# Kernel optimization log

Measured on AMD Instinct MI355X. Metric: run time of the kernel, lower is better.

The kernel has to match this reference:

```python
import jax, jax.numpy as jnp
import numpy as np

DIM = 3072
HEADS = 24
HEAD_DIM = 128
INNER = HEADS * HEAD_DIM
EPS = 1e-6
B, IMG_LEN, TXT_LEN = 1, 2048, 512
S = IMG_LEN + TXT_LEN


def setup_inputs() -> dict:
    key = jax.random.key(0)
    ks = jax.random.split(key, 16)
    w = lambda k, shp: (jax.random.normal(k, shp, dtype=jnp.float32) * 0.02)
    return {
        "x": jax.random.normal(ks[0], (B, IMG_LEN, DIM), dtype=jnp.float32),
        "ctx": jax.random.normal(ks[1], (B, TXT_LEN, DIM), dtype=jnp.float32),
        "rope_cos": jax.random.uniform(ks[2], (S, HEAD_DIM), dtype=jnp.float32),
        "rope_sin": jax.random.uniform(ks[3], (S, HEAD_DIM), dtype=jnp.float32),
        "wq": w(ks[4], (INNER, DIM)),
        "wk": w(ks[5], (INNER, DIM)),
        "wv": w(ks[6], (INNER, DIM)),
        "gq": jnp.ones((HEAD_DIM,), jnp.float32),
        "gk": jnp.ones((HEAD_DIM,), jnp.float32),
        "wo": w(ks[7], (DIM, INNER)),
        "awq": w(ks[8], (INNER, DIM)),
        "awk": w(ks[9], (INNER, DIM)),
        "awv": w(ks[10], (INNER, DIM)),
        "agq": jnp.ones((HEAD_DIM,), jnp.float32),
        "agk": jnp.ones((HEAD_DIM,), jnp.float32),
        "awo": w(ks[11], (DIM, INNER)),
    }


def _rms_norm(t, g):
    # t: [b, s, h, d]; normalize over last dim
    var = jnp.mean(t * t, axis=-1, keepdims=True)
    return t * jax.lax.rsqrt(var + EPS) * g


def _heads(t):
    # [b, s, h*d] -> [b, s, h, d]
    b, s, _ = t.shape
    return t.reshape(b, s, HEADS, HEAD_DIM)


def _apply_rope(t, cos, sin):
    # t: [b, s, h, d]; cos/sin: [s, d] interleaved-pair layout (diffusers Flux style)
    b, s, h, d = t.shape
    x = t.reshape(b, s, h, d // 2, 2)
    rot = jnp.stack([-x[..., 1], x[..., 0]], axis=-1).reshape(b, s, h, d)
    c = cos[None, :, None, :]
    si = sin[None, :, None, :]
    return t * c + rot * si


def reference(x, ctx, rope_cos, rope_sin, wq, wk, wv, gq, gk, wo,
              awq, awk, awv, agq, agk, awo):
    # image-stream QKV + per-head RMSNorm on q,k
    q = _rms_norm(_heads(x @ wq.T), gq)
    k = _rms_norm(_heads(x @ wk.T), gk)
    v = _heads(x @ wv.T)
    # context-stream QKV
    qc = _rms_norm(_heads(ctx @ awq.T), agq)
    kc = _rms_norm(_heads(ctx @ awk.T), agk)
    vc = _heads(ctx @ awv.T)
    # joint streams: [ctx, img] ordering (out[:, :txt_len] is context)
    q = jnp.concatenate([qc, q], axis=1)
    k = jnp.concatenate([kc, k], axis=1)
    v = jnp.concatenate([vc, v], axis=1)
    q = _apply_rope(q, rope_cos, rope_sin)
    k = _apply_rope(k, rope_cos, rope_sin)
    # SDPA
    scale = 1.0 / jnp.sqrt(jnp.float32(HEAD_DIM))
    scores = jnp.einsum('bqhd,bkhd->bhqk', q, k) * scale
    probs = jax.nn.softmax(scores, axis=-1)
    out = jnp.einsum('bhqk,bkhd->bqhd', probs, v)
    out = out.reshape(out.shape[0], out.shape[1], INNER)
    img_out = out[:, TXT_LEN:] @ wo.T
    txt_out = out[:, :TXT_LEN] @ awo.T
    return (img_out, txt_out)
```

## Files before the change

kernel.cpp:

```cpp
#include <hip/hip_runtime.h>
#include <hip/hip_bf16.h>

#define DIMC 3072
#define NHEADS 24
#define HD 128
#define SEQ 2560
#define TXTLEN 512
#define IMGLEN 2048

using short8 = __attribute__((ext_vector_type(8))) short;
using f32x4  = __attribute__((ext_vector_type(4))) float;

static __device__ __forceinline__ float bf2f(unsigned short u) {
    unsigned v = ((unsigned)u) << 16;
    return __builtin_bit_cast(float, v);
}
static __device__ __forceinline__ unsigned short f2bf(float f) {
    unsigned u = __builtin_bit_cast(unsigned, f);
    return (unsigned short)((u + 0x7FFFu + ((u >> 16) & 1u)) >> 16);
}
static __device__ __forceinline__ void gload16(const void* g, void* l) {
    __builtin_amdgcn_global_load_lds((const __attribute__((address_space(1))) unsigned int*)g,
                                     (__attribute__((address_space(3))) unsigned int*)l,
                                     16, 0, 0);
}

__global__ __launch_bounds__(256)
void castk(const float* __restrict__ in, unsigned short* __restrict__ out, int n8)
{
    const int i = blockIdx.x * 256 + threadIdx.x;
    if (i >= n8) return;
    const float4 a = *reinterpret_cast<const float4*>(in + (size_t)i * 8);
    const float4 b = *reinterpret_cast<const float4*>(in + (size_t)i * 8 + 4);
    short8 o;
    o[0] = (short)f2bf(a.x); o[1] = (short)f2bf(a.y);
    o[2] = (short)f2bf(a.z); o[3] = (short)f2bf(a.w);
    o[4] = (short)f2bf(b.x); o[5] = (short)f2bf(b.y);
    o[6] = (short)f2bf(b.z); o[7] = (short)f2bf(b.w);
    *reinterpret_cast<short8*>(out + (size_t)i * 8) = o;
}

struct W8 { const float* src[8]; };
__global__ __launch_bounds__(256)
void castw(W8 a, unsigned short* __restrict__ dstbase, int n8, size_t wsz)
{
    const int i = blockIdx.x * 256 + threadIdx.x;
    if (i >= n8) return;
    const float* in = a.src[blockIdx.y];
    unsigned short* out = dstbase + (size_t)blockIdx.y * wsz;
    const float4 av = *reinterpret_cast<const float4*>(in + (size_t)i * 8);
    const float4 bv = *reinterpret_cast<const float4*>(in + (size_t)i * 8 + 4);
    short8 o;
    o[0] = (short)f2bf(av.x); o[1] = (short)f2bf(av.y);
    o[2] = (short)f2bf(av.z); o[3] = (short)f2bf(av.w);
    o[4] = (short)f2bf(bv.x); o[5] = (short)f2bf(bv.y);
    o[6] = (short)f2bf(bv.z); o[7] = (short)f2bf(bv.w);
    *reinterpret_cast<short8*>(out + (size_t)i * 8) = o;
}

struct QkvArgs {
    const unsigned short* A;
    const unsigned short* w0[3];
    const unsigned short* w1[3];
    unsigned short* c[3];
};

__global__ __launch_bounds__(256)
void gemm_qkv(QkvArgs args)
{
    __shared__ unsigned short As[3][128 * 32];
    __shared__ unsigned short Bs[3][128 * 32];

    const int bid = blockIdx.x;
    const int swz = (bid & 7) * 180 + (bid >> 3);
    const int bm = swz % 20;
    int bn = swz / 20;
    const int which = bn / 24; bn -= which * 24;

    const int rowbase = bm * 128, colbase = bn * 128;
    const unsigned short* __restrict__ A = args.A;
    const unsigned short* __restrict__ W = (rowbase < TXTLEN) ? args.w0[which] : args.w1[which];
    unsigned short* __restrict__ C = args.c[which];

    const int t = threadIdx.x, w = t >> 6, l = t & 63;
    const int lr = l & 15, lk = l >> 4;
    const int wr = (w >> 1) * 64, wc = (w & 1) * 64;

    f32x4 acc[4][4] = {};

    const int ssl = ((l & 3) ^ ((l >> 3) & 3)) * 8;
    const unsigned short* Ag = A + (size_t)(rowbase + w * 32 + (l >> 2)) * DIMC + ssl;
    const unsigned short* Wg = W + (size_t)(colbase + w * 32 + (l >> 2)) * DIMC + ssl;

    auto STAGE = [&](int buf, int k0) {
        gload16(Ag + k0,             &As[buf][w * 1024]);
        gload16(Ag + 16 * DIMC + k0, &As[buf][w * 1024 + 512]);
        gload16(Wg + k0,             &Bs[buf][w * 1024]);
        gload16(Wg + 16 * DIMC + k0, &Bs[buf][w * 1024 + 512]);
    };

    constexpr int NIT = DIMC / 32;
    STAGE(0, 0);
    STAGE(1, 32);

    const int rsl = (lk ^ ((lr >> 1) & 3)) * 8;
    int buf = 0;
    for (int it = 0; it < NIT; ++it) {
        asm volatile("s_waitcnt vmcnt(4)" ::: "memory");
        __builtin_amdgcn_s_barrier();
        asm volatile("" ::: "memory");

        {
            const int k2 = (it + 2 < NIT) ? (it + 2) : (NIT - 1);
            int b2 = buf + 2; if (b2 >= 3) b2 -= 3;
            STAGE(b2, k2 * 32);
        }

        short8 af[4], bf[4];
#pragma unroll
        for (int m = 0; m < 4; ++m)
            af[m] = *reinterpret_cast<const short8*>(&As[buf][(wr + m * 16 + lr) * 32 + rsl]);
#pragma unroll
        for (int n = 0; n < 4; ++n)
            bf[n] = *reinterpret_cast<const short8*>(&Bs[buf][(wc + n * 16 + lr) * 32 + rsl]);

        __builtin_amdgcn_s_setprio(1);
#pragma unroll
        for (int m = 0; m < 4; ++m)
#pragma unroll
            for (int n = 0; n < 4; ++n)
                acc[m][n] = __builtin_amdgcn_mfma_f32_16x16x32_bf16(af[m], bf[n], acc[m][n], 0, 0, 0);
        __builtin_amdgcn_s_setprio(0);

        buf = (buf + 1 == 3) ? 0 : buf + 1;
    }

#pragma unroll
    for (int m = 0; m < 4; ++m) {
#pragma unroll
        for (int r = 0; r < 4; ++r) {
            const int row = rowbase + wr + m * 16 + lk * 4 + r;
            unsigned short* crow = C + (size_t)row * DIMC + colbase + wc;
#pragma unroll
            for (int n = 0; n < 4; ++n)
                crow[n * 16 + lr] = f2bf(acc[m][n][r]);
        }
    }
}

__global__ __launch_bounds__(256)
void gemm_out(const unsigned short* __restrict__ A, const unsigned short* __restrict__ W0,
              const unsigned short* __restrict__ W1, float* __restrict__ Ctxt,
              float* __restrict__ Cimg)
{
    __shared__ unsigned short As[3][128 * 32];
    __shared__ unsigned short Bs[3][128 * 32];

    const int bid = blockIdx.x;
    const int swz = (bid & 7) * 60 + (bid >> 3);
    const int bm = swz % 20;
    const int bn = swz / 20;

    const int rowbase = bm * 128, colbase = bn * 128;
    const unsigned short* __restrict__ W = (rowbase < TXTLEN) ? W0 : W1;

    const int t = threadIdx.x, w = t >> 6, l = t & 63;
    const int lr = l & 15, lk = l >> 4;
    const int wr = (w >> 1) * 64, wc = (w & 1) * 64;

    f32x4 acc[4][4] = {};

    const int ssl = ((l & 3) ^ ((l >> 3) & 3)) * 8;
    const unsigned short* Ag = A + (size_t)(rowbase + w * 32 + (l >> 2)) * DIMC + ssl;
    const unsigned short* Wg = W + (size_t)(colbase + w * 32 + (l >> 2)) * DIMC + ssl;

    auto STAGE = [&](int buf, int k0) {
        gload16(Ag + k0,             &As[buf][w * 1024]);
        gload16(Ag + 16 * DIMC + k0, &As[buf][w * 1024 + 512]);
        gload16(Wg + k0,             &Bs[buf][w * 1024]);
        gload16(Wg + 16 * DIMC + k0, &Bs[buf][w * 1024 + 512]);
    };

    constexpr int NIT = DIMC / 32;
    STAGE(0, 0);
    STAGE(1, 32);

    const int rsl = (lk ^ ((lr >> 1) & 3)) * 8;
    int buf = 0;
    for (int it = 0; it < NIT; ++it) {
        asm volatile("s_waitcnt vmcnt(4)" ::: "memory");
        __builtin_amdgcn_s_barrier();
        asm volatile("" ::: "memory");

        {
            const int k2 = (it + 2 < NIT) ? (it + 2) : (NIT - 1);
            int b2 = buf + 2; if (b2 >= 3) b2 -= 3;
            STAGE(b2, k2 * 32);
        }

        short8 af[4], bf[4];
#pragma unroll
        for (int m = 0; m < 4; ++m)
            af[m] = *reinterpret_cast<const short8*>(&As[buf][(wr + m * 16 + lr) * 32 + rsl]);
#pragma unroll
        for (int n = 0; n < 4; ++n)
            bf[n] = *reinterpret_cast<const short8*>(&Bs[buf][(wc + n * 16 + lr) * 32 + rsl]);

        __builtin_amdgcn_s_setprio(1);
#pragma unroll
        for (int m = 0; m < 4; ++m)
#pragma unroll
            for (int n = 0; n < 4; ++n)
                acc[m][n] = __builtin_amdgcn_mfma_f32_16x16x32_bf16(af[m], bf[n], acc[m][n], 0, 0, 0);
        __builtin_amdgcn_s_setprio(0);

        buf = (buf + 1 == 3) ? 0 : buf + 1;
    }

    float* Cb; int rloc;
    if (rowbase < TXTLEN) { Cb = Ctxt; rloc = rowbase; }
    else                  { Cb = Cimg; rloc = rowbase - TXTLEN; }
#pragma unroll
    for (int m = 0; m < 4; ++m) {
#pragma unroll
        for (int r = 0; r < 4; ++r) {
            const int row = rloc + wr + m * 16 + lk * 4 + r;
            float* crow = Cb + (size_t)row * DIMC + colbase + wc;
#pragma unroll
            for (int n = 0; n < 4; ++n)
                crow[n * 16 + lr] = acc[m][n][r];
        }
    }
}

__global__ __launch_bounds__(256)
void normrope(unsigned short* __restrict__ Q, unsigned short* __restrict__ K,
              const float* __restrict__ gq, const float* __restrict__ gk,
              const float* __restrict__ agq, const float* __restrict__ agk,
              const float* __restrict__ rc, const float* __restrict__ rs)
{
    const int wid  = (blockIdx.x << 2) + (threadIdx.x >> 6);
    const int lane = threadIdx.x & 63;
    const int s = wid / NHEADS, h = wid - s * NHEADS;
    const bool img = (s >= TXTLEN);
    const float* gq_ = img ? gq : agq;
    const float* gk_ = img ? gk : agk;

    const size_t base = (size_t)s * DIMC + h * HD + lane * 2;
    const float2 c2  = *reinterpret_cast<const float2*>(rc + (size_t)s * HD + lane * 2);
    const float2 s2  = *reinterpret_cast<const float2*>(rs + (size_t)s * HD + lane * 2);
    const float2 gqv = *reinterpret_cast<const float2*>(gq_ + lane * 2);
    const float2 gkv = *reinterpret_cast<const float2*>(gk_ + lane * 2);

    {
        unsigned pr = *reinterpret_cast<unsigned*>(Q + base);
        float vx = bf2f((unsigned short)(pr & 0xffff));
        float vy = bf2f((unsigned short)(pr >> 16));
        float ss = vx * vx + vy * vy;
#pragma unroll
        for (int off = 1; off < 64; off <<= 1) ss += __shfl_xor(ss, off);
        const float rr = rsqrtf(ss * (1.f / HD) + 1e-6f);
        const float txv = vx * rr * gqv.x, tyv = vy * rr * gqv.y;
        const float qs = 0.08838834764831845f;
        const float ox = (txv * c2.x - tyv * s2.x) * qs;
        const float oy = (tyv * c2.y + txv * s2.y) * qs;
        *reinterpret_cast<unsigned*>(Q + base) = (unsigned)f2bf(ox) | ((unsigned)f2bf(oy) << 16);
    }
    {
        unsigned pr = *reinterpret_cast<unsigned*>(K + base);
        float vx = bf2f((unsigned short)(pr & 0xffff));
        float vy = bf2f((unsigned short)(pr >> 16));
        float ss = vx * vx + vy * vy;
#pragma unroll
        for (int off = 1; off < 64; off <<= 1) ss += __shfl_xor(ss, off);
        const float rr = rsqrtf(ss * (1.f / HD) + 1e-6f);
        const float txv = vx * rr * gkv.x, tyv = vy * rr * gkv.y;
        const float ox = txv * c2.x - tyv * s2.x;
        const float oy = tyv * c2.y + txv * s2.y;
        *reinterpret_cast<unsigned*>(K + base) = (unsigned)f2bf(ox) | ((unsigned)f2bf(oy) << 16);
    }
}

__global__ __launch_bounds__(256)
void transpose_v(const unsigned short* __restrict__ V, unsigned short* __restrict__ Vt)
{
    __shared__ unsigned short Ts[64][136];
    const int kt = blockIdx.x, h = blockIdx.y;
    const int t = threadIdx.x;
#pragma unroll
    for (int p = 0; p < 4; ++p) {
        const int row = p * 16 + (t >> 4);
        const int col = (t & 15) * 8;
        *reinterpret_cast<short8*>(&Ts[row][col]) =
            *reinterpret_cast<const short8*>(V + (size_t)(kt * 64 + row) * DIMC + h * HD + col);
    }
    __syncthreads();
    const int d = t >> 1, kh = t & 1;
    unsigned short* dst = Vt + (size_t)h * HD * SEQ + (size_t)d * SEQ + kt * 64 + kh * 32;
#pragma unroll
    for (int j4 = 0; j4 < 4; ++j4) {
        short8 o;
#pragma unroll
        for (int j = 0; j < 8; ++j) o[j] = (short)Ts[kh * 32 + j4 * 8 + j][d];
        *reinterpret_cast<short8*>(dst + j4 * 8) = o;
    }
}

__global__ __launch_bounds__(512)
void attn_mfma(const unsigned short* __restrict__ Q, const unsigned short* __restrict__ K,
               const unsigned short* __restrict__ Vt, unsigned short* __restrict__ O)
{
    __shared__ unsigned short Ks[2][64 * 128];
    __shared__ unsigned short Vs[2][128 * 64];
    __shared__ unsigned short Ps[8][16 * 64];

    const int bid = blockIdx.x;
    const int swz = (bid & 7) * 60 + (bid >> 3);
    const int bq = swz % 20;
    const int h  = swz / 20;

    const int t = threadIdx.x, w = t >> 6, l = t & 63;
    const int lr = l & 15, lk = l >> 4;
    const int q0 = bq * 128 + w * 16;

    short8 qf[4];
#pragma unroll
    for (int kk = 0; kk < 4; ++kk)
        qf[kk] = *reinterpret_cast<const short8*>(
            Q + (size_t)(q0 + lr) * DIMC + h * HD + kk * 32 + lk * 8);

    f32x4 oacc[8] = {};
    float mrow[4] = {-1e30f, -1e30f, -1e30f, -1e30f};
    float lrow[4] = {};

    const unsigned short* Kg[2];
    const unsigned short* Vg[2];
#pragma unroll
    for (int i = 0; i < 2; ++i) {
        const int kr = w * 8 + i * 4 + (l >> 4);
        Kg[i] = K + (size_t)kr * DIMC + h * HD + (((l & 15) ^ (kr & 7)) * 8);
        const int vr = w * 16 + i * 8 + (l >> 3);
        Vg[i] = Vt + (size_t)h * HD * SEQ + (size_t)vr * SEQ + (((l & 7) ^ (vr & 7)) * 8);
    }

    auto STAGE = [&](int buf, int kv0) {
#pragma unroll
        for (int i = 0; i < 2; ++i) {
            gload16(Kg[i] + (size_t)kv0 * DIMC, &Ks[buf][(w * 8 + i * 4) * 128]);
            gload16(Vg[i] + kv0,                &Vs[buf][(w * 16 + i * 8) * 64]);
        }
    };

    STAGE(0, 0);

    constexpr int NT = SEQ / 64;
    for (int kt = 0; kt < NT; ++kt) {
        const int buf = kt & 1;
        __syncthreads();
        if (kt + 1 < NT) STAGE(buf ^ 1, (kt + 1) * 64);

        f32x4 sf[4] = {};
        __builtin_amdgcn_s_setprio(1);
#pragma unroll
        for (int nf = 0; nf < 4; ++nf) {
            const int row = nf * 16 + lr;
            const int sw = (row & 7) << 3;
#pragma unroll
            for (int kk = 0; kk < 4; ++kk) {
                short8 bfr = *reinterpret_cast<const short8*>(
                    &Ks[buf][row * 128 + ((kk * 32 + lk * 8) ^ sw)]);
                sf[nf] = __builtin_amdgcn_mfma_f32_16x16x32_bf16(qf[kk], bfr, sf[nf], 0, 0, 0);
            }
        }
        __builtin_amdgcn_s_setprio(0);

        float mxr[4];
#pragma unroll
        for (int r = 0; r < 4; ++r) {
            float mx = fmaxf(fmaxf(sf[0][r], sf[1][r]), fmaxf(sf[2][r], sf[3][r]));
#pragma unroll
            for (int off = 1; off < 16; off <<= 1) mx = fmaxf(mx, __shfl_xor(mx, off));
            mxr[r] = mx;
        }
        const float need = fmaxf(fmaxf(mxr[0] - mrow[0], mxr[1] - mrow[1]),
                                 fmaxf(mxr[2] - mrow[2], mxr[3] - mrow[3]));
        if (!__all(need <= 8.0f)) {
#pragma unroll
            for (int r = 0; r < 4; ++r) {
                const float mn = fmaxf(mrow[r], mxr[r]);
                const float alpha = __expf(mrow[r] - mn);
                mrow[r] = mn;
                lrow[r] *= alpha;
#pragma unroll
                for (int nf = 0; nf < 8; ++nf) oacc[nf][r] *= alpha;
            }
        }
#pragma unroll
        for (int r = 0; r < 4; ++r) {
            float ps = 0.f;
#pragma unroll
            for (int nf = 0; nf < 4; ++nf) {
                const float p = __expf(sf[nf][r] - mrow[r]);
                sf[nf][r] = p;
                ps += p;
            }
#pragma unroll
            for (int off = 1; off < 16; off <<= 1) ps += __shfl_xor(ps, off);
            lrow[r] += ps;
        }

#pragma unroll
        for (int r = 0; r < 4; ++r) {
            const int prow = lk * 4 + r;
            const int sw = (prow & 7) << 3;
#pragma unroll
            for (int nf = 0; nf < 4; ++nf) {
                const int col = nf * 16 + lr;
                Ps[w][prow * 64 + (col ^ sw)] = f2bf(sf[nf][r]);
            }
        }

        __builtin_amdgcn_s_setprio(1);
#pragma unroll
        for (int ks = 0; ks < 2; ++ks) {
            short8 pa = *reinterpret_cast<const short8*>(
                &Ps[w][lr * 64 + ((ks * 32 + lk * 8) ^ ((lr & 7) << 3))]);
#pragma unroll
            for (int nf = 0; nf < 8; ++nf) {
                const int vrow = nf * 16 + lr;
                short8 vf = *reinterpret_cast<const short8*>(
                    &Vs[buf][vrow * 64 + ((ks * 32 + lk * 8) ^ ((vrow & 7) << 3))]);
                oacc[nf] = __builtin_amdgcn_mfma_f32_16x16x32_bf16(pa, vf, oacc[nf], 0, 0, 0);
            }
        }
        __builtin_amdgcn_s_setprio(0);
    }

    float inv[4];
#pragma unroll
    for (int r = 0; r < 4; ++r) inv[r] = 1.f / lrow[r];
#pragma unroll
    for (int nf = 0; nf < 8; ++nf)
#pragma unroll
        for (int r = 0; r < 4; ++r)
            O[(size_t)(q0 + lk * 4 + r) * DIMC + h * HD + nf * 16 + lr] = f2bf(oacc[nf][r] * inv[r]);
}

extern "C" void kernel_launch(void* const* d_in, const int* in_sizes, int n_in,
                              void* d_out, int out_size, void* d_ws, size_t ws_size,
                              hipStream_t stream)
{
    const float* x    = (const float*)d_in[0];
    const float* ctx  = (const float*)d_in[1];
    const float* rc   = (const float*)d_in[2];
    const float* rs   = (const float*)d_in[3];
    const float* wq   = (const float*)d_in[4];
    const float* wk   = (const float*)d_in[5];
    const float* wv   = (const float*)d_in[6];
    const float* gq   = (const float*)d_in[7];
    const float* gk   = (const float*)d_in[8];
    const float* wo   = (const float*)d_in[9];
    const float* awq  = (const float*)d_in[10];
    const float* awk  = (const float*)d_in[11];
    const float* awv  = (const float*)d_in[12];
    const float* agq  = (const float*)d_in[13];
    const float* agk  = (const float*)d_in[14];
    const float* awo  = (const float*)d_in[15];

    unsigned short* wsp = (unsigned short*)d_ws;
    const size_t SZ  = (size_t)SEQ * DIMC;
    const size_t WSZ = (size_t)DIMC * DIMC;
    unsigned short* XC  = wsp;
    unsigned short* Qb  = XC + SZ;
    unsigned short* Kb  = Qb + SZ;
    unsigned short* Vb  = Kb + SZ;
    unsigned short* Vtb = Vb + SZ;
    unsigned short* Ob  = Vtb + SZ;
    unsigned short* Wc  = Ob + SZ;

    {
        int n8 = (int)((size_t)TXTLEN * DIMC / 8);
        castk<<<dim3((n8 + 255) / 256), dim3(256), 0, stream>>>(ctx, XC, n8);
        n8 = (int)((size_t)IMGLEN * DIMC / 8);
        castk<<<dim3((n8 + 255) / 256), dim3(256), 0, stream>>>(x, XC + (size_t)TXTLEN * DIMC, n8);
    }
    {
        W8 w8;
        w8.src[0] = awq; w8.src[1] = wq; w8.src[2] = awk; w8.src[3] = wk;
        w8.src[4] = awv; w8.src[5] = wv; w8.src[6] = awo; w8.src[7] = wo;
        const int n8 = (int)(WSZ / 8);
        castw<<<dim3((n8 + 255) / 256, 8), dim3(256), 0, stream>>>(w8, Wc, n8, WSZ);
    }

    QkvArgs qa;
    qa.A = XC;
    qa.w0[0] = Wc + 0 * WSZ; qa.w1[0] = Wc + 1 * WSZ; qa.c[0] = Qb;
    qa.w0[1] = Wc + 2 * WSZ; qa.w1[1] = Wc + 3 * WSZ; qa.c[1] = Kb;
    qa.w0[2] = Wc + 4 * WSZ; qa.w1[2] = Wc + 5 * WSZ; qa.c[2] = Vb;
    gemm_qkv<<<dim3(1440), dim3(256), 0, stream>>>(qa);

    normrope<<<dim3(SEQ * NHEADS / 4), dim3(256), 0, stream>>>(Qb, Kb, gq, gk, agq, agk, rc, rs);

    transpose_v<<<dim3(SEQ / 64, NHEADS), dim3(256), 0, stream>>>(Vb, Vtb);

    attn_mfma<<<dim3(480), dim3(512), 0, stream>>>(Qb, Kb, Vtb, Ob);

    float* out = (float*)d_out;
    gemm_out<<<dim3(480), dim3(256), 0, stream>>>(
        Ob, Wc + 6 * WSZ, Wc + 7 * WSZ, out + (size_t)IMGLEN * DIMC, out);
}
```

Baseline: 535.2 us.

## Retile QKV GEMM to 256x192 blocks with 512 threads and split-phase pipelining

Rewrites the QKV projection GEMM to use 256x192 output tiles, 64-wide K steps and 8 waves per block, so each wave holds a 128x48 accumulator. Shared memory becomes a double buffer, and A/B tile loads are spread across four sub-phases of each K tile so loads overlap with MFMA work. The larger tiles raise arithmetic intensity and cut global traffic per output. The cost is more registers and LDS per block, and 480 blocks give a less even tail across CUs.

```diff
diff --git a/kernel.cpp b/kernel.cpp
--- a/kernel.cpp
+++ b/kernel.cpp
@@ -65,85 +65,128 @@
     unsigned short* c[3];
 };
 
-__global__ __launch_bounds__(256)
+__global__ __launch_bounds__(512)
 void gemm_qkv(QkvArgs args)
 {
-    __shared__ unsigned short As[3][128 * 32];
-    __shared__ unsigned short Bs[3][128 * 32];
+    __shared__ unsigned short As[2][256 * 64];
+    __shared__ unsigned short Bs[2][192 * 64];
 
     const int bid = blockIdx.x;
-    const int swz = (bid & 7) * 180 + (bid >> 3);
-    const int bm = swz % 20;
-    int bn = swz / 20;
-    const int which = bn / 24; bn -= which * 24;
-
-    const int rowbase = bm * 128, colbase = bn * 128;
+    const int swz = (bid & 7) * 60 + (bid >> 3);
+    const int which = swz / 160;
+    const int rem = swz - which * 160;
+    const int bn = rem / 10;
+    const int bm = rem - bn * 10;
+
+    const int rowbase = bm * 256, colbase = bn * 192;
     const unsigned short* __restrict__ A = args.A;
     const unsigned short* __restrict__ W = (rowbase < TXTLEN) ? args.w0[which] : args.w1[which];
     unsigned short* __restrict__ C = args.c[which];
 
-    const int t = threadIdx.x, w = t >> 6, l = t & 63;
+    const int t = threadIdx.x, l = t & 63;
+    const int w = t >> 6;
     const int lr = l & 15, lk = l >> 4;
-    const int wr = (w >> 1) * 64, wc = (w & 1) * 64;
-
-    f32x4 acc[4][4] = {};
-
-    const int ssl = ((l & 3) ^ ((l >> 3) & 3)) * 8;
-    const unsigned short* Ag = A + (size_t)(rowbase + w * 32 + (l >> 2)) * DIMC + ssl;
-    const unsigned short* Wg = W + (size_t)(colbase + w * 32 + (l >> 2)) * DIMC + ssl;
-
-    auto STAGE = [&](int buf, int k0) {
-        gload16(Ag + k0,             &As[buf][w * 1024]);
-        gload16(Ag + 16 * DIMC + k0, &As[buf][w * 1024 + 512]);
-        gload16(Wg + k0,             &Bs[buf][w * 1024]);
-        gload16(Wg + 16 * DIMC + k0, &Bs[buf][w * 1024 + 512]);
+    const int wm = w >> 2, wn = w & 3;
+
+    f32x4 acc[8][3] = {};
+
+    const int srow = t >> 3;
+    const int gsl  = ((t & 7) ^ (srow & 7)) * 8;
+    const int dst0 = srow * 64 + (t & 7) * 8;
+
+    const unsigned short* AgR[4];
+    const unsigned short* WgR[3];
+#pragma unroll
+    for (int r = 0; r < 4; ++r)
+        AgR[r] = A + (size_t)(rowbase + r * 64 + srow) * DIMC + gsl;
+#pragma unroll
+    for (int r = 0; r < 3; ++r)
+        WgR[r] = W + (size_t)(colbase + r * 64 + srow) * DIMC + gsl;
+
+    auto SA2 = [&](unsigned short* dst, int r, int k0) {
+        gload16(AgR[r] + k0, dst + r * 4096 + dst0);
     };
-
-    constexpr int NIT = DIMC / 32;
-    STAGE(0, 0);
-    STAGE(1, 32);
-
-    const int rsl = (lk ^ ((lr >> 1) & 3)) * 8;
-    int buf = 0;
-    for (int it = 0; it < NIT; ++it) {
-        asm volatile("s_waitcnt vmcnt(4)" ::: "memory");
-        __builtin_amdgcn_s_barrier();
-        asm volatile("" ::: "memory");
-
-        {
-            const int k2 = (it + 2 < NIT) ? (it + 2) : (NIT - 1);
-            int b2 = buf + 2; if (b2 >= 3) b2 -= 3;
-            STAGE(b2, k2 * 32);
-        }
-
-        short8 af[4], bf[4];
-#pragma unroll
-        for (int m = 0; m < 4; ++m)
-            af[m] = *reinterpret_cast<const short8*>(&As[buf][(wr + m * 16 + lr) * 32 + rsl]);
-#pragma unroll
-        for (int n = 0; n < 4; ++n)
-            bf[n] = *reinterpret_cast<const short8*>(&Bs[buf][(wc + n * 16 + lr) * 32 + rsl]);
-
-        __builtin_amdgcn_s_setprio(1);
-#pragma unroll
-        for (int m = 0; m < 4; ++m)
-#pragma unroll
-            for (int n = 0; n < 4; ++n)
-                acc[m][n] = __builtin_amdgcn_mfma_f32_16x16x32_bf16(af[m], bf[n], acc[m][n], 0, 0, 0);
-        __builtin_amdgcn_s_setprio(0);
-
-        buf = (buf + 1 == 3) ? 0 : buf + 1;
-    }
-
-#pragma unroll
-    for (int m = 0; m < 4; ++m) {
+    auto SB2 = [&](unsigned short* dst, int r, int k0) {
+        gload16(WgR[r] + k0, dst + r * 4096 + dst0);
+    };
+
+    const int xsl0 = ((lk)     ^ (lr & 7)) * 8;
+    const int xsl1 = ((lk + 4) ^ (lr & 7)) * 8;
+    const int arow = wm * 128 + lr;
+    const int brow = wn * 48 + lr;
+
+    constexpr int NT = DIMC / 64;
+    constexpr int ITERS = NT / 2;
+
+#pragma unroll
+    for (int r = 0; r < 4; ++r) SA2(&As[0][0], r, 0);
+#pragma unroll
+    for (int r = 0; r < 3; ++r) SB2(&Bs[0][0], r, 0);
+#pragma unroll
+    for (int r = 0; r < 3; ++r) SB2(&Bs[1][0], r, 64);
+
+    auto HALF = [&](int CB, int kA, int kB) {
+        unsigned short* Ab  = &As[CB][0];
+        unsigned short* Bb  = &Bs[CB][0];
+        unsigned short* Aot = &As[CB ^ 1][0];
+        short8 bfr[3][2];
+#pragma unroll
+        for (int q = 0; q < 4; ++q) {
+            if (q == 0) {
+                asm volatile("s_waitcnt vmcnt(3)" ::: "memory");
+            }
+            __builtin_amdgcn_s_barrier();
+            if (q == 0) {
+#pragma unroll
+                for (int nf = 0; nf < 3; ++nf) {
+                    bfr[nf][0] = *reinterpret_cast<const short8*>(&Bb[(brow + nf * 16) * 64 + xsl0]);
+                    bfr[nf][1] = *reinterpret_cast<const short8*>(&Bb[(brow + nf * 16) * 64 + xsl1]);
+                }
+            }
+            short8 afr[2][2];
+#pragma unroll
+            for (int i = 0; i < 2; ++i) {
+                afr[i][0] = *reinterpret_cast<const short8*>(&Ab[(arow + (2 * q + i) * 16) * 64 + xsl0]);
+                afr[i][1] = *reinterpret_cast<const short8*>(&Ab[(arow + (2 * q + i) * 16) * 64 + xsl1]);
+            }
+            if (q == 0)      { SA2(Aot, 0, kA); SA2(Aot, 1, kA); }
+            else if (q == 1) { SA2(Aot, 2, kA); SA2(Aot, 3, kA); }
+            else if (q == 2) { SB2(Bb,  0, kB); SB2(Bb,  1, kB); }
+            else             { SB2(Bb,  2, kB); }
+
+            __builtin_amdgcn_s_setprio(1);
+#pragma unroll
+            for (int i = 0; i < 2; ++i)
+#pragma unroll
+                for (int nf = 0; nf < 3; ++nf) {
+                    acc[2 * q + i][nf] = __builtin_amdgcn_mfma_f32_16x16x32_bf16(
+                        afr[i][0], bfr[nf][0], acc[2 * q + i][nf], 0, 0, 0);
+                    acc[2 * q + i][nf] = __builtin_amdgcn_mfma_f32_16x16x32_bf16(
+                        afr[i][1], bfr[nf][1], acc[2 * q + i][nf], 0, 0, 0);
+                }
+            __builtin_amdgcn_s_setprio(0);
+        }
+    };
+
+    for (int it = 0; it < ITERS; ++it) {
+        const int t2 = 2 * it + 2 < NT ? 2 * it + 2 : NT - 1;
+        const int t3 = 2 * it + 3 < NT ? 2 * it + 3 : NT - 1;
+        HALF(0, (2 * it + 1) * 64, t2 * 64);
+        HALF(1, t2 * 64,           t3 * 64);
+    }
+
+    asm volatile("s_waitcnt vmcnt(0)" ::: "memory");
+    __builtin_amdgcn_s_barrier();
+
+#pragma unroll
+    for (int mf = 0; mf < 8; ++mf) {
 #pragma unroll
         for (int r = 0; r < 4; ++r) {
-            const int row = rowbase + wr + m * 16 + lk * 4 + r;
-            unsigned short* crow = C + (size_t)row * DIMC + colbase + wc;
-#pragma unroll
-            for (int n = 0; n < 4; ++n)
-                crow[n * 16 + lr] = f2bf(acc[m][n][r]);
+            const int row = rowbase + wm * 128 + mf * 16 + lk * 4 + r;
+            unsigned short* crow = C + (size_t)row * DIMC + colbase + wn * 48;
+#pragma unroll
+            for (int nf = 0; nf < 3; ++nf)
+                crow[nf * 16 + lr] = f2bf(acc[mf][nf][r]);
         }
     }
 }
@@ -497,7 +540,7 @@
     qa.w0[0] = Wc + 0 * WSZ; qa.w1[0] = Wc + 1 * WSZ; qa.c[0] = Qb;
     qa.w0[1] = Wc + 2 * WSZ; qa.w1[1] = Wc + 3 * WSZ; qa.c[1] = Kb;
     qa.w0[2] = Wc + 4 * WSZ; qa.w1[2] = Wc + 5 * WSZ; qa.c[2] = Vb;
-    gemm_qkv<<<dim3(1440), dim3(256), 0, stream>>>(qa);
+    gemm_qkv<<<dim3(480), dim3(512), 0, stream>>>(qa);
 
     normrope<<<dim3(SEQ * NHEADS / 4), dim3(256), 0, stream>>>(Qb, Kb, gq, gk, agq, agk, rc, rs);
 
```

Measured after the change: 537.0 us. About the same (+0.3%).

## Fuse fp32-to-bf16 weight conversion into GEMM B-tile staging

Applied to the files above, without the earlier changes.

Removes the separate kernel that cast all eight fp32 weight matrices to bf16 in a workspace. The QKV and output GEMMs now read fp32 weights straight into registers, convert them to bf16, and write them into the swizzled shared-memory B tiles, while the A tiles still use direct global-to-LDS loads. This cuts a large extra read-and-write pass over the weights and one kernel launch. In exchange, each weight tile is read at twice the width by every row block, conversion ALU work is added to the main loop, and register-loaded weights force the memory wait earlier, which weakens the three-buffer prefetch overlap.

```diff
diff --git a/kernel.cpp b/kernel.cpp
--- a/kernel.cpp
+++ b/kernel.cpp
@@ -40,28 +40,10 @@
     *reinterpret_cast<short8*>(out + (size_t)i * 8) = o;
 }
 
-struct W8 { const float* src[8]; };
-__global__ __launch_bounds__(256)
-void castw(W8 a, unsigned short* __restrict__ dstbase, int n8, size_t wsz)
-{
-    const int i = blockIdx.x * 256 + threadIdx.x;
-    if (i >= n8) return;
-    const float* in = a.src[blockIdx.y];
-    unsigned short* out = dstbase + (size_t)blockIdx.y * wsz;
-    const float4 av = *reinterpret_cast<const float4*>(in + (size_t)i * 8);
-    const float4 bv = *reinterpret_cast<const float4*>(in + (size_t)i * 8 + 4);
-    short8 o;
-    o[0] = (short)f2bf(av.x); o[1] = (short)f2bf(av.y);
-    o[2] = (short)f2bf(av.z); o[3] = (short)f2bf(av.w);
-    o[4] = (short)f2bf(bv.x); o[5] = (short)f2bf(bv.y);
-    o[6] = (short)f2bf(bv.z); o[7] = (short)f2bf(bv.w);
-    *reinterpret_cast<short8*>(out + (size_t)i * 8) = o;
-}
-
 struct QkvArgs {
     const unsigned short* A;
-    const unsigned short* w0[3];
-    const unsigned short* w1[3];
+    const float* w0[3];
+    const float* w1[3];
     unsigned short* c[3];
 };
 
@@ -79,7 +61,7 @@
 
     const int rowbase = bm * 128, colbase = bn * 128;
     const unsigned short* __restrict__ A = args.A;
-    const unsigned short* __restrict__ W = (rowbase < TXTLEN) ? args.w0[which] : args.w1[which];
+    const float* __restrict__ W = (rowbase < TXTLEN) ? args.w0[which] : args.w1[which];
     unsigned short* __restrict__ C = args.c[which];
 
     const int t = threadIdx.x, w = t >> 6, l = t & 63;
@@ -90,31 +72,60 @@
 
     const int ssl = ((l & 3) ^ ((l >> 3) & 3)) * 8;
     const unsigned short* Ag = A + (size_t)(rowbase + w * 32 + (l >> 2)) * DIMC + ssl;
-    const unsigned short* Wg = W + (size_t)(colbase + w * 32 + (l >> 2)) * DIMC + ssl;
-
-    auto STAGE = [&](int buf, int k0) {
+
+    const float* Wg = W + (size_t)(colbase + w * 32 + (l >> 2)) * DIMC + (l & 3) * 8;
+    const int wa0 = (w * 32 + (l >> 2)) * 32 + ssl;
+    const int wa1 = wa0 + 512;
+
+    auto STAGE_A = [&](int buf, int k0) {
         gload16(Ag + k0,             &As[buf][w * 1024]);
         gload16(Ag + 16 * DIMC + k0, &As[buf][w * 1024 + 512]);
-        gload16(Wg + k0,             &Bs[buf][w * 1024]);
-        gload16(Wg + 16 * DIMC + k0, &Bs[buf][w * 1024 + 512]);
+    };
+    auto LOADW = [&](int k0, float4& a, float4& b, float4& c2, float4& d) {
+        a  = *reinterpret_cast<const float4*>(Wg + k0);
+        b  = *reinterpret_cast<const float4*>(Wg + k0 + 4);
+        c2 = *reinterpret_cast<const float4*>(Wg + 16 * DIMC + k0);
+        d  = *reinterpret_cast<const float4*>(Wg + 16 * DIMC + k0 + 4);
+    };
+    auto CVTW = [&](int buf, float4 a, float4 b, float4 c2, float4 d) {
+        short8 s0, s1;
+        s0[0] = (short)f2bf(a.x);  s0[1] = (short)f2bf(a.y);
+        s0[2] = (short)f2bf(a.z);  s0[3] = (short)f2bf(a.w);
+        s0[4] = (short)f2bf(b.x);  s0[5] = (short)f2bf(b.y);
+        s0[6] = (short)f2bf(b.z);  s0[7] = (short)f2bf(b.w);
+        s1[0] = (short)f2bf(c2.x); s1[1] = (short)f2bf(c2.y);
+        s1[2] = (short)f2bf(c2.z); s1[3] = (short)f2bf(c2.w);
+        s1[4] = (short)f2bf(d.x);  s1[5] = (short)f2bf(d.y);
+        s1[6] = (short)f2bf(d.z);  s1[7] = (short)f2bf(d.w);
+        *reinterpret_cast<short8*>(&Bs[buf][wa0]) = s0;
+        *reinterpret_cast<short8*>(&Bs[buf][wa1]) = s1;
     };
 
     constexpr int NIT = DIMC / 32;
-    STAGE(0, 0);
-    STAGE(1, 32);
+
+    {
+        float4 v0, v1, v2, v3, u0, u1, u2, u3;
+        LOADW(0, v0, v1, v2, v3);
+        STAGE_A(0, 0);
+        LOADW(32, u0, u1, u2, u3);
+        STAGE_A(1, 32);
+        CVTW(0, v0, v1, v2, v3);
+        CVTW(1, u0, u1, u2, u3);
+    }
 
     const int rsl = (lk ^ ((lr >> 1) & 3)) * 8;
     int buf = 0;
     for (int it = 0; it < NIT; ++it) {
-        asm volatile("s_waitcnt vmcnt(4)" ::: "memory");
+        asm volatile("s_waitcnt lgkmcnt(0)" ::: "memory");
         __builtin_amdgcn_s_barrier();
         asm volatile("" ::: "memory");
 
-        {
-            const int k2 = (it + 2 < NIT) ? (it + 2) : (NIT - 1);
-            int b2 = buf + 2; if (b2 >= 3) b2 -= 3;
-            STAGE(b2, k2 * 32);
-        }
+        const int k2 = ((it + 2 < NIT) ? it + 2 : NIT - 1) * 32;
+        int b2 = buf + 2; if (b2 >= 3) b2 -= 3;
+        float4 a0, a1, a2, a3;
+        LOADW(k2, a0, a1, a2, a3);
+        asm volatile("" ::: "memory");
+        STAGE_A(b2, k2);
 
         short8 af[4], bf[4];
 #pragma unroll
@@ -132,8 +143,13 @@
                 acc[m][n] = __builtin_amdgcn_mfma_f32_16x16x32_bf16(af[m], bf[n], acc[m][n], 0, 0, 0);
         __builtin_amdgcn_s_setprio(0);
 
+        CVTW(b2, a0, a1, a2, a3);
+
         buf = (buf + 1 == 3) ? 0 : buf + 1;
     }
+
+    asm volatile("s_waitcnt vmcnt(0) lgkmcnt(0)" ::: "memory");
+    __builtin_amdgcn_s_barrier();
 
 #pragma unroll
     for (int m = 0; m < 4; ++m) {
@@ -149,8 +165,8 @@
 }
 
 __global__ __launch_bounds__(256)
-void gemm_out(const unsigned short* __restrict__ A, const unsigned short* __restrict__ W0,
-              const unsigned short* __restrict__ W1, float* __restrict__ Ctxt,
+void gemm_out(const unsigned short* __restrict__ A, const float* __restrict__ W0,
+              const float* __restrict__ W1, float* __restrict__ Ctxt,
               float* __restrict__ Cimg)
 {
     __shared__ unsigned short As[3][128 * 32];
@@ -162,7 +178,7 @@
     const int bn = swz / 20;
 
     const int rowbase = bm * 128, colbase = bn * 128;
-    const unsigned short* __restrict__ W = (rowbase < TXTLEN) ? W0 : W1;
+    const float* __restrict__ W = (rowbase < TXTLEN) ? W0 : W1;
 
     const int t = threadIdx.x, w = t >> 6, l = t & 63;
     const int lr = l & 15, lk = l >> 4;
@@ -172,31 +188,59 @@
 
     const int ssl = ((l & 3) ^ ((l >> 3) & 3)) * 8;
     const unsigned short* Ag = A + (size_t)(rowbase + w * 32 + (l >> 2)) * DIMC + ssl;
-    const unsigned short* Wg = W + (size_t)(colbase + w * 32 + (l >> 2)) * DIMC + ssl;
-
-    auto STAGE = [&](int buf, int k0) {
+    const float* Wg = W + (size_t)(colbase + w * 32 + (l >> 2)) * DIMC + (l & 3) * 8;
+    const int wa0 = (w * 32 + (l >> 2)) * 32 + ssl;
+    const int wa1 = wa0 + 512;
+
+    auto STAGE_A = [&](int buf, int k0) {
         gload16(Ag + k0,             &As[buf][w * 1024]);
         gload16(Ag + 16 * DIMC + k0, &As[buf][w * 1024 + 512]);
-        gload16(Wg + k0,             &Bs[buf][w * 1024]);
-        gload16(Wg + 16 * DIMC + k0, &Bs[buf][w * 1024 + 512]);
+    };
+    auto LOADW = [&](int k0, float4& a, float4& b, float4& c2, float4& d) {
+        a  = *reinterpret_cast<const float4*>(Wg + k0);
+        b  = *reinterpret_cast<const float4*>(Wg + k0 + 4);
+        c2 = *reinterpret_cast<const float4*>(Wg + 16 * DIMC + k0);
+        d  = *reinterpret_cast<const float4*>(Wg + 16 * DIMC + k0 + 4);
+    };
+    auto CVTW = [&](int buf, float4 a, float4 b, float4 c2, float4 d) {
+        short8 s0, s1;
+        s0[0] = (short)f2bf(a.x);  s0[1] = (short)f2bf(a.y);
+        s0[2] = (short)f2bf(a.z);  s0[3] = (short)f2bf(a.w);
+        s0[4] = (short)f2bf(b.x);  s0[5] = (short)f2bf(b.y);
+        s0[6] = (short)f2bf(b.z);  s0[7] = (short)f2bf(b.w);
+        s1[0] = (short)f2bf(c2.x); s1[1] = (short)f2bf(c2.y);
+        s1[2] = (short)f2bf(c2.z); s1[3] = (short)f2bf(c2.w);
+        s1[4] = (short)f2bf(d.x);  s1[5] = (short)f2bf(d.y);
+        s1[6] = (short)f2bf(d.z);  s1[7] = (short)f2bf(d.w);
+        *reinterpret_cast<short8*>(&Bs[buf][wa0]) = s0;
+        *reinterpret_cast<short8*>(&Bs[buf][wa1]) = s1;
     };
 
     constexpr int NIT = DIMC / 32;
-    STAGE(0, 0);
-    STAGE(1, 32);
+
+    {
+        float4 v0, v1, v2, v3, u0, u1, u2, u3;
+        LOADW(0, v0, v1, v2, v3);
+        STAGE_A(0, 0);
+        LOADW(32, u0, u1, u2, u3);
+        STAGE_A(1, 32);
+        CVTW(0, v0, v1, v2, v3);
+        CVTW(1, u0, u1, u2, u3);
+    }
 
     const int rsl = (lk ^ ((lr >> 1) & 3)) * 8;
     int buf = 0;
     for (int it = 0; it < NIT; ++it) {
-        asm volatile("s_waitcnt vmcnt(4)" ::: "memory");
+        asm volatile("s_waitcnt lgkmcnt(0)" ::: "memory");
         __builtin_amdgcn_s_barrier();
         asm volatile("" ::: "memory");
 
-        {
-            const int k2 = (it + 2 < NIT) ? (it + 2) : (NIT - 1);
-            int b2 = buf + 2; if (b2 >= 3) b2 -= 3;
-            STAGE(b2, k2 * 32);
-        }
+        const int k2 = ((it + 2 < NIT) ? it + 2 : NIT - 1) * 32;
+        int b2 = buf + 2; if (b2 >= 3) b2 -= 3;
+        float4 a0, a1, a2, a3;
+        LOADW(k2, a0, a1, a2, a3);
+        asm volatile("" ::: "memory");
+        STAGE_A(b2, k2);
 
         short8 af[4], bf[4];
 #pragma unroll
@@ -214,8 +258,13 @@
                 acc[m][n] = __builtin_amdgcn_mfma_f32_16x16x32_bf16(af[m], bf[n], acc[m][n], 0, 0, 0);
         __builtin_amdgcn_s_setprio(0);
 
+        CVTW(b2, a0, a1, a2, a3);
+
         buf = (buf + 1 == 3) ? 0 : buf + 1;
     }
+
+    asm volatile("s_waitcnt vmcnt(0) lgkmcnt(0)" ::: "memory");
+    __builtin_amdgcn_s_barrier();
 
     float* Cb; int rloc;
     if (rowbase < TXTLEN) { Cb = Ctxt; rloc = rowbase; }
@@ -469,14 +518,12 @@
 
     unsigned short* wsp = (unsigned short*)d_ws;
     const size_t SZ  = (size_t)SEQ * DIMC;
-    const size_t WSZ = (size_t)DIMC * DIMC;
     unsigned short* XC  = wsp;
     unsigned short* Qb  = XC + SZ;
     unsigned short* Kb  = Qb + SZ;
     unsigned short* Vb  = Kb + SZ;
     unsigned short* Vtb = Vb + SZ;
     unsigned short* Ob  = Vtb + SZ;
-    unsigned short* Wc  = Ob + SZ;
 
     {
         int n8 = (int)((size_t)TXTLEN * DIMC / 8);
@@ -484,19 +531,12 @@
         n8 = (int)((size_t)IMGLEN * DIMC / 8);
         castk<<<dim3((n8 + 255) / 256), dim3(256), 0, stream>>>(x, XC + (size_t)TXTLEN * DIMC, n8);
     }
-    {
-        W8 w8;
-        w8.src[0] = awq; w8.src[1] = wq; w8.src[2] = awk; w8.src[3] = wk;
-        w8.src[4] = awv; w8.src[5] = wv; w8.src[6] = awo; w8.src[7] = wo;
-        const int n8 = (int)(WSZ / 8);
-        castw<<<dim3((n8 + 255) / 256, 8), dim3(256), 0, stream>>>(w8, Wc, n8, WSZ);
-    }
 
     QkvArgs qa;
     qa.A = XC;
-    qa.w0[0] = Wc + 0 * WSZ; qa.w1[0] = Wc + 1 * WSZ; qa.c[0] = Qb;
-    qa.w0[1] = Wc + 2 * WSZ; qa.w1[1] = Wc + 3 * WSZ; qa.c[1] = Kb;
-    qa.w0[2] = Wc + 4 * WSZ; qa.w1[2] = Wc + 5 * WSZ; qa.c[2] = Vb;
+    qa.w0[0] = awq; qa.w1[0] = wq; qa.c[0] = Qb;
+    qa.w0[1] = awk; qa.w1[1] = wk; qa.c[1] = Kb;
+    qa.w0[2] = awv; qa.w1[2] = wv; qa.c[2] = Vb;
     gemm_qkv<<<dim3(1440), dim3(256), 0, stream>>>(qa);
 
     normrope<<<dim3(SEQ * NHEADS / 4), dim3(256), 0, stream>>>(Qb, Kb, gq, gk, agq, agk, rc, rs);
@@ -507,5 +547,5 @@
 
     float* out = (float*)d_out;
     gemm_out<<<dim3(480), dim3(256), 0, stream>>>(
-        Ob, Wc + 6 * WSZ, Wc + 7 * WSZ, out + (size_t)IMGLEN * DIMC, out);
-}
+        Ob, awo, wo, out + (size_t)IMGLEN * DIMC, out);
+}
```

Result: slower. 582.4 us (+8.8%).
